# Kernel optimization log

Hardware: AMD Instinct MI355X
Metric: run time of the kernel (lower is better)

The kernel has to match this reference:

```python
import jax, jax.numpy as jnp
import numpy as np

TEMPERATURE = 8.0  # sqrt(d_k=64)


def setup_inputs() -> dict:
    key = jax.random.key(0)
    kq, kk, kv = jax.random.split(key, 3)
    B, H, L, D = 4, 16, 2048, 64
    q = jax.random.normal(kq, (B, H, L, D), dtype=jnp.float32)
    k = jax.random.normal(kk, (B, H, L, D), dtype=jnp.float32)
    v = jax.random.normal(kv, (B, H, L, D), dtype=jnp.float32)
    return {"q": q, "k": k, "v": v}


def reference(q, k, v):
    # attn = softmax((q/T) @ k^T)  over last axis; dropout is identity in eval
    scores = jnp.einsum("bhqd,bhkd->bhqk", q / TEMPERATURE, k)
    attn = jax.nn.softmax(scores, axis=-1)
    out = jnp.einsum("bhqk,bhkd->bhqd", attn, v)
    return (out, attn)
```

## Files before the change

kernel.cpp:

```cpp
#include <hip/hip_runtime.h>
#include <hip/hip_bf16.h>

typedef __attribute__((ext_vector_type(4))) float  f32x4;
typedef __attribute__((ext_vector_type(8))) short  bf16x8;
typedef __attribute__((ext_vector_type(4))) short  bf16x4;

#define MFMA16(a, b, c) __builtin_amdgcn_mfma_f32_16x16x32_bf16((a), (b), (c), 0, 0, 0)

__device__ __forceinline__ short f2bf(float f) {
  return __builtin_bit_cast(short, __float2bfloat16(f));
}
__device__ __forceinline__ float bf2f(short b) {
  return __builtin_bit_cast(float, ((unsigned)(unsigned short)b) << 16);
}

__device__ __forceinline__ void sync_lds() {
  asm volatile("s_waitcnt lgkmcnt(0)" ::: "memory");
  __builtin_amdgcn_s_barrier();
  asm volatile("" ::: "memory");
}

constexpr int L = 2048, D = 64, KT = 64, NT = L / KT;
constexpr int NHEAD = 64;
constexpr int QB = 128, NQT = L / QB;
constexpr float QSCALE = 0.18033688011112042f;
constexpr size_t WS_NEED = (size_t)3 * NHEAD * L * D * sizeof(short);

__global__ __launch_bounds__(256)
void sdpa_prep(const float* __restrict__ Q, const float* __restrict__ K,
               const float* __restrict__ V,
               short* __restrict__ Qb, short* __restrict__ Kb,
               short* __restrict__ Vtb)
{
  __shared__ short Tl[64 * 72];
  const int t = threadIdx.x;
  const int head = blockIdx.x >> 5, kt = blockIdx.x & 31;
  const long base = (long)head * L * D + (long)kt * 64 * D;

  {
    const float* qp = Q + base + t * 16;
    short*       qo = Qb + base + t * 16;
    bf16x8 y0, y1;
    #pragma unroll
    for (int j = 0; j < 8; ++j) {
      y0[j] = f2bf(qp[j]     * QSCALE);
      y1[j] = f2bf(qp[8 + j] * QSCALE);
    }
    *(bf16x8*)qo = y0; *(bf16x8*)(qo + 8) = y1;
  }
  {
    const float* kp = K + base + t * 16;
    short*       ko = Kb + base + t * 16;
    bf16x8 y0, y1;
    #pragma unroll
    for (int j = 0; j < 8; ++j) { y0[j] = f2bf(kp[j]); y1[j] = f2bf(kp[8 + j]); }
    *(bf16x8*)ko = y0; *(bf16x8*)(ko + 8) = y1;
  }
  {
    const int kr0 = (t >> 4) * 4, d0 = (t & 15) * 4;
    const float* vp = V + base;
    f32x4 r[4];
    #pragma unroll
    for (int i = 0; i < 4; ++i) r[i] = *(const f32x4*)(vp + (kr0 + i) * D + d0);
    #pragma unroll
    for (int j = 0; j < 4; ++j) {
      bf16x4 y;
      #pragma unroll
      for (int i = 0; i < 4; ++i) y[i] = f2bf(r[i][j]);
      *(bf16x4*)(&Tl[(d0 + j) * 72 + kr0]) = y;
    }
  }
  __syncthreads();
  {
    const int d = t >> 2, k0 = (t & 3) * 16;
    bf16x8 a = *(const bf16x8*)(&Tl[d * 72 + k0]);
    bf16x8 b = *(const bf16x8*)(&Tl[d * 72 + k0 + 8]);
    short* vo = Vtb + (long)head * D * L + (long)d * L + kt * 64 + k0;
    *(bf16x8*)vo = a; *(bf16x8*)(vo + 8) = b;
  }
}

__global__ __launch_bounds__(256, 4)
void sdpa_main(const short* __restrict__ Qb, const short* __restrict__ Kb,
               const short* __restrict__ Vtb, float* __restrict__ out,
               float* __restrict__ attn)
{
  __shared__ short Klds[2][KT * D];
  __shared__ short Vlds[2][D * KT];
  __shared__ short Plds[4][16 * KT];

  const int t = threadIdx.x, lane = t & 63, w = t >> 6;
  const int qr = lane & 15, g = lane >> 4;

  const int bid = blockIdx.x;
  const int wid = ((bid & 7) << 7) | (bid >> 3);
  const int head = wid >> 4, qt = wid & 15;
  const long hoff = (long)head * L * D;
  const int qrow0 = qt * QB + w * 32;

  bf16x8 qfrag[2][2];
  #pragma unroll
  for (int h = 0; h < 2; ++h) {
    const short* qbp = Qb + hoff + (long)(qrow0 + 16 * h + qr) * D + g * 8;
    qfrag[h][0] = *(const bf16x8*)qbp;
    qfrag[h][1] = *(const bf16x8*)(qbp + 32);
  }

  const short* Kbase = Kb + hoff;
  const short* Vbase = Vtb + (long)head * D * L;

  bf16x8 kreg[2], vreg[2];
  const int krow = t >> 2, kd0 = (t & 3) * 16;

  auto loadK = [&](int kt) {
    const short* kp = Kbase + (long)(kt * KT + krow) * D + kd0;
    kreg[0] = *(const bf16x8*)kp;
    kreg[1] = *(const bf16x8*)(kp + 8);
  };
  auto writeK = [&](int buf) {
    const int sw = (krow & 7) << 3;
    *(bf16x8*)(&Klds[buf][krow * 64 + (kd0 ^ sw)])       = kreg[0];
    *(bf16x8*)(&Klds[buf][krow * 64 + ((kd0 + 8) ^ sw)]) = kreg[1];
  };
  auto loadV = [&](int kt) {
    const short* vp = Vbase + (long)krow * L + kt * KT + kd0;
    vreg[0] = *(const bf16x8*)vp;
    vreg[1] = *(const bf16x8*)(vp + 8);
  };
  auto writeV = [&](int buf) {
    const int sw = (krow & 7) << 3;
    *(bf16x8*)(&Vlds[buf][krow * 64 + (kd0 ^ sw)])       = vreg[0];
    *(bf16x8*)(&Vlds[buf][krow * 64 + ((kd0 + 8) ^ sw)]) = vreg[1];
  };

  auto computeS2 = [&](int buf, f32x4 s0[4], f32x4 s1[4]) {
    #pragma unroll
    for (int f = 0; f < 4; ++f) {
      s0[f] = (f32x4){0.f, 0.f, 0.f, 0.f};
      s1[f] = (f32x4){0.f, 0.f, 0.f, 0.f};
      int kr = f * 16 + qr;
      #pragma unroll
      for (int c = 0; c < 2; ++c) {
        int d0c = g * 8 + 32 * c;
        bf16x8 a = *(const bf16x8*)(&Klds[buf][kr * 64 + (d0c ^ ((kr & 7) << 3))]);
        s0[f] = MFMA16(a, qfrag[0][c], s0[f]);
        s1[f] = MFMA16(a, qfrag[1][c], s1[f]);
      }
    }
  };

  loadK(0); writeK(0);
  sync_lds();
  float rsum0 = 0.f, rsum1 = 0.f;
  for (int kt = 0; kt < NT; ++kt) {
    const int cur = kt & 1;
    if (kt + 1 < NT) loadK(kt + 1);
    f32x4 s0[4], s1[4];
    computeS2(cur, s0, s1);
    #pragma unroll
    for (int f = 0; f < 4; ++f)
      #pragma unroll
      for (int r = 0; r < 4; ++r) {
        rsum0 += __builtin_amdgcn_exp2f(s0[f][r]);
        rsum1 += __builtin_amdgcn_exp2f(s1[f][r]);
      }
    if (kt + 1 < NT) writeK(cur ^ 1);
    sync_lds();
  }
  rsum0 += __shfl_xor(rsum0, 16); rsum0 += __shfl_xor(rsum0, 32);
  rsum1 += __shfl_xor(rsum1, 16); rsum1 += __shfl_xor(rsum1, 32);
  const float rinv0 = 1.f / rsum0;
  const float rinv1 = 1.f / rsum1;

  f32x4 o0[4] = {{0.f,0.f,0.f,0.f},{0.f,0.f,0.f,0.f},{0.f,0.f,0.f,0.f},{0.f,0.f,0.f,0.f}};
  f32x4 o1[4] = {{0.f,0.f,0.f,0.f},{0.f,0.f,0.f,0.f},{0.f,0.f,0.f,0.f},{0.f,0.f,0.f,0.f}};
  float* ap0 = attn + (long)head * L * L + (long)(qrow0 + qr) * L;
  float* ap1 = ap0 + 16 * L;

  auto doHalf = [&](f32x4 s[4], float rinv, float* ap, f32x4 o[4], int cur, int kt) {
    #pragma unroll
    for (int f = 0; f < 4; ++f) {
      f32x4 pf;
      #pragma unroll
      for (int r = 0; r < 4; ++r)
        pf[r] = __builtin_amdgcn_exp2f(s[f][r]) * rinv;
      *(f32x4*)(ap + kt * KT + f * 16 + g * 4) = pf;
      bf16x4 p;
      #pragma unroll
      for (int r = 0; r < 4; ++r) p[r] = f2bf(pf[r]);
      int k0 = f * 16 + g * 4;
      *(bf16x4*)(&Plds[w][qr * 64 + (k0 ^ ((qr & 7) << 3))]) = p;
    }
    __builtin_amdgcn_wave_barrier();
    #pragma unroll
    for (int kc = 0; kc < 2; ++kc) {
      int k0 = kc * 32 + g * 8;
      bf16x8 pa = *(const bf16x8*)(&Plds[w][qr * 64 + (k0 ^ ((qr & 7) << 3))]);
      #pragma unroll
      for (int fr = 0; fr < 4; ++fr) {
        int d = fr * 16 + qr;
        bf16x8 vb = *(const bf16x8*)(&Vlds[cur][d * 64 + (k0 ^ ((d & 7) << 3))]);
        o[fr] = MFMA16(pa, vb, o[fr]);
      }
    }
    __builtin_amdgcn_wave_barrier();
  };

  loadK(0); loadV(0);
  writeK(0); writeV(0);
  sync_lds();

  for (int kt = 0; kt < NT; ++kt) {
    const int cur = kt & 1;
    if (kt + 1 < NT) { loadK(kt + 1); loadV(kt + 1); }

    f32x4 s0[4], s1[4];
    computeS2(cur, s0, s1);

    doHalf(s0, rinv0, ap0, o0, cur, kt);
    doHalf(s1, rinv1, ap1, o1, cur, kt);

    if (kt + 1 < NT) { writeK(cur ^ 1); writeV(cur ^ 1); }
    sync_lds();
  }

  float* op = out + hoff + (long)qrow0 * D;
  #pragma unroll
  for (int fr = 0; fr < 4; ++fr)
    #pragma unroll
    for (int r = 0; r < 4; ++r) {
      op[(long)(g * 4 + r) * D + fr * 16 + qr]      = o0[fr][r];
      op[(long)(16 + g * 4 + r) * D + fr * 16 + qr] = o1[fr][r];
    }
}

__global__ __launch_bounds__(256, 4)
void sdpa_fused(const float* __restrict__ Q, const float* __restrict__ K,
                const float* __restrict__ V, float* __restrict__ out,
                float* __restrict__ attn)
{
  __shared__ short Klds[2][KT * D];
  __shared__ short Vlds[2][D * KT];
  __shared__ short Plds[4][16 * KT];

  const int t = threadIdx.x, lane = t & 63, w = t >> 6;
  const int qr = lane & 15, g = lane >> 4;
  const int head = blockIdx.x >> 5, qt = blockIdx.x & 31;
  const long hoff = (long)head * L * D;
  const int qrow0 = qt * 64 + w * 16;

  bf16x8 qfrag[2];
  {
    const float* qp = Q + hoff + (long)(qrow0 + qr) * D + g * 8;
    #pragma unroll
    for (int c = 0; c < 2; ++c)
      #pragma unroll
      for (int j = 0; j < 8; ++j)
        qfrag[c][j] = f2bf(qp[32 * c + j] * QSCALE);
  }

  const float* Kbase = K + hoff;
  const float* Vbase = V + hoff;
  f32x4 kreg[4], vreg[4];

  auto loadK = [&](int kt) {
    const float* kp = Kbase + (long)kt * KT * D;
    #pragma unroll
    for (int c = 0; c < 4; ++c)
      kreg[c] = *(const f32x4*)(kp + (t + 256 * c) * 4);
  };
  auto writeK = [&](int buf) {
    #pragma unroll
    for (int c = 0; c < 4; ++c) {
      int f = t + 256 * c;
      int kr = f >> 4, col = (f & 15) * 4;
      bf16x4 y;
      #pragma unroll
      for (int i = 0; i < 4; ++i) y[i] = f2bf(kreg[c][i]);
      *(bf16x4*)(&Klds[buf][kr * 64 + (col ^ ((kr & 7) << 3))]) = y;
    }
  };
  auto loadV = [&](int kt) {
    const float* vp = Vbase + (long)kt * KT * D;
    int kr0 = (t >> 4) * 4, d0 = (t & 15) * 4;
    #pragma unroll
    for (int i = 0; i < 4; ++i)
      vreg[i] = *(const f32x4*)(vp + (kr0 + i) * D + d0);
  };
  auto writeV = [&](int buf) {
    int kr0 = (t >> 4) * 4, d0 = (t & 15) * 4;
    #pragma unroll
    for (int j = 0; j < 4; ++j) {
      bf16x4 y;
      #pragma unroll
      for (int i = 0; i < 4; ++i) y[i] = f2bf(vreg[i][j]);
      int d = d0 + j;
      *(bf16x4*)(&Vlds[buf][d * 64 + (kr0 ^ ((d & 7) << 3))]) = y;
    }
  };
  auto computeS = [&](int buf, f32x4 s[4]) {
    #pragma unroll
    for (int f = 0; f < 4; ++f) {
      s[f] = (f32x4){0.f, 0.f, 0.f, 0.f};
      int kr = f * 16 + qr;
      #pragma unroll
      for (int c = 0; c < 2; ++c) {
        int d0c = g * 8 + 32 * c;
        bf16x8 a = *(const bf16x8*)(&Klds[buf][kr * 64 + (d0c ^ ((kr & 7) << 3))]);
        s[f] = MFMA16(a, qfrag[c], s[f]);
      }
    }
  };

  loadK(0); writeK(0);
  sync_lds();
  float rsum = 0.f;
  for (int kt = 0; kt < NT; ++kt) {
    const int cur = kt & 1;
    if (kt + 1 < NT) loadK(kt + 1);
    f32x4 s[4];
    computeS(cur, s);
    #pragma unroll
    for (int f = 0; f < 4; ++f)
      #pragma unroll
      for (int r = 0; r < 4; ++r)
        rsum += __builtin_amdgcn_exp2f(s[f][r]);
    if (kt + 1 < NT) writeK(cur ^ 1);
    sync_lds();
  }
  rsum += __shfl_xor(rsum, 16);
  rsum += __shfl_xor(rsum, 32);
  const float rinv = 1.f / rsum;

  f32x4 o[4] = {{0.f,0.f,0.f,0.f},{0.f,0.f,0.f,0.f},{0.f,0.f,0.f,0.f},{0.f,0.f,0.f,0.f}};
  float* ap_base = attn + (long)head * L * L + (long)qrow0 * L;

  loadK(0); loadV(0);
  writeK(0); writeV(0);
  sync_lds();

  for (int kt = 0; kt < NT; ++kt) {
    const int cur = kt & 1;
    if (kt + 1 < NT) { loadK(kt + 1); loadV(kt + 1); }

    f32x4 s[4];
    computeS(cur, s);

    #pragma unroll
    for (int f = 0; f < 4; ++f) {
      bf16x4 p;
      #pragma unroll
      for (int r = 0; r < 4; ++r)
        p[r] = f2bf(__builtin_amdgcn_exp2f(s[f][r]) * rinv);
      int k0 = f * 16 + g * 4;
      *(bf16x4*)(&Plds[w][qr * 64 + (k0 ^ ((qr & 7) << 3))]) = p;
    }
    __builtin_amdgcn_wave_barrier();

    float* ap = ap_base + (long)kt * KT;
    #pragma unroll
    for (int i = 0; i < 4; ++i) {
      int r = 4 * i + g, col = 4 * qr;
      bf16x4 pb = *(const bf16x4*)(&Plds[w][r * 64 + (col ^ ((r & 7) << 3))]);
      f32x4 pf;
      #pragma unroll
      for (int j = 0; j < 4; ++j) pf[j] = bf2f(pb[j]);
      *(f32x4*)(ap + (long)r * L + col) = pf;
    }

    #pragma unroll
    for (int kc = 0; kc < 2; ++kc) {
      int k0 = kc * 32 + g * 8;
      bf16x8 pa = *(const bf16x8*)(&Plds[w][qr * 64 + (k0 ^ ((qr & 7) << 3))]);
      #pragma unroll
      for (int fr = 0; fr < 4; ++fr) {
        int d = fr * 16 + qr;
        bf16x8 vb = *(const bf16x8*)(&Vlds[cur][d * 64 + (k0 ^ ((d & 7) << 3))]);
        o[fr] = MFMA16(pa, vb, o[fr]);
      }
    }

    if (kt + 1 < NT) { writeK(cur ^ 1); writeV(cur ^ 1); }
    sync_lds();
  }

  float* op = out + hoff + (long)qrow0 * D;
  #pragma unroll
  for (int fr = 0; fr < 4; ++fr)
    #pragma unroll
    for (int r = 0; r < 4; ++r) {
      int qq = g * 4 + r;
      op[(long)qq * D + fr * 16 + qr] = o[fr][r];
    }
}

extern "C" void kernel_launch(void* const* d_in, const int* in_sizes, int n_in,
                              void* d_out, int out_size, void* d_ws, size_t ws_size,
                              hipStream_t stream) {
  const float* q = (const float*)d_in[0];
  const float* k = (const float*)d_in[1];
  const float* v = (const float*)d_in[2];
  float* out  = (float*)d_out;
  float* attn = (float*)d_out + (size_t)NHEAD * L * D;

  dim3 block(256);

  if (ws_size >= WS_NEED) {
    short* Qb  = (short*)d_ws;
    short* Kb  = Qb + (size_t)NHEAD * L * D;
    short* Vtb = Kb + (size_t)NHEAD * L * D;
    hipLaunchKernelGGL(sdpa_prep, dim3(NHEAD * NT), block, 0, stream, q, k, v, Qb, Kb, Vtb);
    hipLaunchKernelGGL(sdpa_main, dim3(NHEAD * NQT), block, 0, stream, Qb, Kb, Vtb, out, attn);
  } else {
    hipLaunchKernelGGL(sdpa_fused, dim3(NHEAD * NT), block, 0, stream, q, k, v, out, attn);
  }
}
```

Before: 352.1 us.

## Split softmax row-sum pass into separate kernel writing reciprocals to workspace

Moves the first pass, which computes the exp-sum of QK^T per row, out of the main attention kernel into its own kernel. That kernel uses only a K LDS buffer and writes 1/rowsum per query row to workspace, and the main kernel reads these values back. The goal is to give each kernel lower LDS and register pressure, which could raise occupancy. In exchange it adds a kernel launch, reloads Q and K in the new kernel, and needs a larger workspace, so the fast path is skipped when less workspace is provided.

```diff
diff --git a/kernel.cpp b/kernel.cpp
--- a/kernel.cpp
+++ b/kernel.cpp
@@ -24,7 +24,8 @@
 constexpr int NHEAD = 64;
 constexpr int QB = 128, NQT = L / QB;
 constexpr float QSCALE = 0.18033688011112042f;
-constexpr size_t WS_NEED = (size_t)3 * NHEAD * L * D * sizeof(short);
+constexpr size_t BF_ELEMS = (size_t)NHEAD * L * D;
+constexpr size_t WS_NEED = 3 * BF_ELEMS * sizeof(short) + (size_t)NHEAD * L * sizeof(float);
 
 __global__ __launch_bounds__(256)
 void sdpa_prep(const float* __restrict__ Q, const float* __restrict__ K,
@@ -81,13 +82,10 @@
 }
 
 __global__ __launch_bounds__(256, 4)
-void sdpa_main(const short* __restrict__ Qb, const short* __restrict__ Kb,
-               const short* __restrict__ Vtb, float* __restrict__ out,
-               float* __restrict__ attn)
+void sdpa_rowsum(const short* __restrict__ Qb, const short* __restrict__ Kb,
+                 float* __restrict__ rinv_out)
 {
   __shared__ short Klds[2][KT * D];
-  __shared__ short Vlds[2][D * KT];
-  __shared__ short Plds[4][16 * KT];
 
   const int t = threadIdx.x, lane = t & 63, w = t >> 6;
   const int qr = lane & 15, g = lane >> 4;
@@ -107,9 +105,7 @@
   }
 
   const short* Kbase = Kb + hoff;
-  const short* Vbase = Vtb + (long)head * D * L;
-
-  bf16x8 kreg[2], vreg[2];
+  bf16x8 kreg[2];
   const int krow = t >> 2, kd0 = (t & 3) * 16;
 
   auto loadK = [&](int kt) {
@@ -121,32 +117,6 @@
     const int sw = (krow & 7) << 3;
     *(bf16x8*)(&Klds[buf][krow * 64 + (kd0 ^ sw)])       = kreg[0];
     *(bf16x8*)(&Klds[buf][krow * 64 + ((kd0 + 8) ^ sw)]) = kreg[1];
-  };
-  auto loadV = [&](int kt) {
-    const short* vp = Vbase + (long)krow * L + kt * KT + kd0;
-    vreg[0] = *(const bf16x8*)vp;
-    vreg[1] = *(const bf16x8*)(vp + 8);
-  };
-  auto writeV = [&](int buf) {
-    const int sw = (krow & 7) << 3;
-    *(bf16x8*)(&Vlds[buf][krow * 64 + (kd0 ^ sw)])       = vreg[0];
-    *(bf16x8*)(&Vlds[buf][krow * 64 + ((kd0 + 8) ^ sw)]) = vreg[1];
-  };
-
-  auto computeS2 = [&](int buf, f32x4 s0[4], f32x4 s1[4]) {
-    #pragma unroll
-    for (int f = 0; f < 4; ++f) {
-      s0[f] = (f32x4){0.f, 0.f, 0.f, 0.f};
-      s1[f] = (f32x4){0.f, 0.f, 0.f, 0.f};
-      int kr = f * 16 + qr;
-      #pragma unroll
-      for (int c = 0; c < 2; ++c) {
-        int d0c = g * 8 + 32 * c;
-        bf16x8 a = *(const bf16x8*)(&Klds[buf][kr * 64 + (d0c ^ ((kr & 7) << 3))]);
-        s0[f] = MFMA16(a, qfrag[0][c], s0[f]);
-        s1[f] = MFMA16(a, qfrag[1][c], s1[f]);
-      }
-    }
   };
 
   loadK(0); writeK(0);
@@ -155,22 +125,107 @@
   for (int kt = 0; kt < NT; ++kt) {
     const int cur = kt & 1;
     if (kt + 1 < NT) loadK(kt + 1);
-    f32x4 s0[4], s1[4];
-    computeS2(cur, s0, s1);
-    #pragma unroll
-    for (int f = 0; f < 4; ++f)
+    #pragma unroll
+    for (int f = 0; f < 4; ++f) {
+      f32x4 s0 = (f32x4){0.f,0.f,0.f,0.f};
+      f32x4 s1 = (f32x4){0.f,0.f,0.f,0.f};
+      int kr = f * 16 + qr;
+      #pragma unroll
+      for (int c = 0; c < 2; ++c) {
+        int d0c = g * 8 + 32 * c;
+        bf16x8 a = *(const bf16x8*)(&Klds[cur][kr * 64 + (d0c ^ ((kr & 7) << 3))]);
+        s0 = MFMA16(a, qfrag[0][c], s0);
+        s1 = MFMA16(a, qfrag[1][c], s1);
+      }
       #pragma unroll
       for (int r = 0; r < 4; ++r) {
-        rsum0 += __builtin_amdgcn_exp2f(s0[f][r]);
-        rsum1 += __builtin_amdgcn_exp2f(s1[f][r]);
-      }
+        rsum0 += __builtin_amdgcn_exp2f(s0[r]);
+        rsum1 += __builtin_amdgcn_exp2f(s1[r]);
+      }
+    }
     if (kt + 1 < NT) writeK(cur ^ 1);
     sync_lds();
   }
   rsum0 += __shfl_xor(rsum0, 16); rsum0 += __shfl_xor(rsum0, 32);
   rsum1 += __shfl_xor(rsum1, 16); rsum1 += __shfl_xor(rsum1, 32);
-  const float rinv0 = 1.f / rsum0;
-  const float rinv1 = 1.f / rsum1;
+  if (lane < 16) {
+    float* ro = rinv_out + (long)head * L + qrow0;
+    ro[qr]      = 1.f / rsum0;
+    ro[16 + qr] = 1.f / rsum1;
+  }
+}
+
+__global__ __launch_bounds__(256, 4)
+void sdpa_main(const short* __restrict__ Qb, const short* __restrict__ Kb,
+               const short* __restrict__ Vtb, const float* __restrict__ rinv_ws,
+               float* __restrict__ out, float* __restrict__ attn)
+{
+  __shared__ short Klds[2][KT * D];
+  __shared__ short Vlds[2][D * KT];
+  __shared__ short Plds[4][16 * KT];
+
+  const int t = threadIdx.x, lane = t & 63, w = t >> 6;
+  const int qr = lane & 15, g = lane >> 4;
+
+  const int bid = blockIdx.x;
+  const int wid = ((bid & 7) << 7) | (bid >> 3);
+  const int head = wid >> 4, qt = wid & 15;
+  const long hoff = (long)head * L * D;
+  const int qrow0 = qt * QB + w * 32;
+
+  const float rinv0 = rinv_ws[(long)head * L + qrow0 + qr];
+  const float rinv1 = rinv_ws[(long)head * L + qrow0 + 16 + qr];
+
+  bf16x8 qfrag[2][2];
+  #pragma unroll
+  for (int h = 0; h < 2; ++h) {
+    const short* qbp = Qb + hoff + (long)(qrow0 + 16 * h + qr) * D + g * 8;
+    qfrag[h][0] = *(const bf16x8*)qbp;
+    qfrag[h][1] = *(const bf16x8*)(qbp + 32);
+  }
+
+  const short* Kbase = Kb + hoff;
+  const short* Vbase = Vtb + (long)head * D * L;
+
+  bf16x8 kreg[2], vreg[2];
+  const int krow = t >> 2, kd0 = (t & 3) * 16;
+
+  auto loadK = [&](int kt) {
+    const short* kp = Kbase + (long)(kt * KT + krow) * D + kd0;
+    kreg[0] = *(const bf16x8*)kp;
+    kreg[1] = *(const bf16x8*)(kp + 8);
+  };
+  auto writeK = [&](int buf) {
+    const int sw = (krow & 7) << 3;
+    *(bf16x8*)(&Klds[buf][krow * 64 + (kd0 ^ sw)])       = kreg[0];
+    *(bf16x8*)(&Klds[buf][krow * 64 + ((kd0 + 8) ^ sw)]) = kreg[1];
+  };
+  auto loadV = [&](int kt) {
+    const short* vp = Vbase + (long)krow * L + kt * KT + kd0;
+    vreg[0] = *(const bf16x8*)vp;
+    vreg[1] = *(const bf16x8*)(vp + 8);
+  };
+  auto writeV = [&](int buf) {
+    const int sw = (krow & 7) << 3;
+    *(bf16x8*)(&Vlds[buf][krow * 64 + (kd0 ^ sw)])       = vreg[0];
+    *(bf16x8*)(&Vlds[buf][krow * 64 + ((kd0 + 8) ^ sw)]) = vreg[1];
+  };
+
+  auto computeS2 = [&](int buf, f32x4 s0[4], f32x4 s1[4]) {
+    #pragma unroll
+    for (int f = 0; f < 4; ++f) {
+      s0[f] = (f32x4){0.f, 0.f, 0.f, 0.f};
+      s1[f] = (f32x4){0.f, 0.f, 0.f, 0.f};
+      int kr = f * 16 + qr;
+      #pragma unroll
+      for (int c = 0; c < 2; ++c) {
+        int d0c = g * 8 + 32 * c;
+        bf16x8 a = *(const bf16x8*)(&Klds[buf][kr * 64 + (d0c ^ ((kr & 7) << 3))]);
+        s0[f] = MFMA16(a, qfrag[0][c], s0[f]);
+        s1[f] = MFMA16(a, qfrag[1][c], s1[f]);
+      }
+    }
+  };
 
   f32x4 o0[4] = {{0.f,0.f,0.f,0.f},{0.f,0.f,0.f,0.f},{0.f,0.f,0.f,0.f},{0.f,0.f,0.f,0.f}};
   f32x4 o1[4] = {{0.f,0.f,0.f,0.f},{0.f,0.f,0.f,0.f},{0.f,0.f,0.f,0.f},{0.f,0.f,0.f,0.f}};
@@ -406,11 +461,13 @@
   dim3 block(256);
 
   if (ws_size >= WS_NEED) {
-    short* Qb  = (short*)d_ws;
-    short* Kb  = Qb + (size_t)NHEAD * L * D;
-    short* Vtb = Kb + (size_t)NHEAD * L * D;
-    hipLaunchKernelGGL(sdpa_prep, dim3(NHEAD * NT), block, 0, stream, q, k, v, Qb, Kb, Vtb);
-    hipLaunchKernelGGL(sdpa_main, dim3(NHEAD * NQT), block, 0, stream, Qb, Kb, Vtb, out, attn);
+    short* Qb   = (short*)d_ws;
+    short* Kb   = Qb + BF_ELEMS;
+    short* Vtb  = Kb + BF_ELEMS;
+    float* rinv = (float*)(Vtb + BF_ELEMS);
+    hipLaunchKernelGGL(sdpa_prep,   dim3(NHEAD * NT),  block, 0, stream, q, k, v, Qb, Kb, Vtb);
+    hipLaunchKernelGGL(sdpa_rowsum, dim3(NHEAD * NQT), block, 0, stream, Qb, Kb, rinv);
+    hipLaunchKernelGGL(sdpa_main,   dim3(NHEAD * NQT), block, 0, stream, Qb, Kb, Vtb, rinv, out, attn);
   } else {
     hipLaunchKernelGGL(sdpa_fused, dim3(NHEAD * NT), block, 0, stream, q, k, v, out, attn);
   }
```

Measured after the change: 354.2 us. Within noise of the previous version (+0.6%).
